# Performance work log

Measured on AMD Instinct MI355X. Metric: run time of the kernel, lower is better.

The kernel has to match this reference:

```python
import jax, jax.numpy as jnp
import numpy as np

N_NODES = 50000
N_EDGES = 1600000
IN_DIM = 64
HEADS = 8
DHEAD = 8  # out_dim per head
CLAMP = 5.0


def _xavier(key, shape):
    # xavier_normal_ for a torch Linear weight [out, in]; we store transposed [in, out]
    fan_in, fan_out = shape[0], shape[1]
    std = np.sqrt(2.0 / (fan_in + fan_out))
    return jax.random.normal(key, shape, jnp.float32) * jnp.float32(std)


def setup_inputs() -> dict:
    key = jax.random.key(0)
    ks = jax.random.split(key, 8)
    x = jax.random.normal(ks[0], (N_NODES, IN_DIM), jnp.float32)
    edge_attr = jax.random.normal(ks[1], (N_EDGES, IN_DIM), jnp.float32)
    edge_index = jax.random.randint(ks[2], (2, N_EDGES), 0, N_NODES)
    HD = HEADS * DHEAD
    WQ = _xavier(ks[3], (IN_DIM, HD)); bQ = jnp.zeros((HD,), jnp.float32)
    WK = _xavier(ks[4], (IN_DIM, HD))  # use_bias=False -> no bias for K
    WV = _xavier(ks[5], (IN_DIM, HD))  # no bias for V
    WE1 = _xavier(ks[6], (IN_DIM, HD)); bE1 = jnp.zeros((HD,), jnp.float32)
    return {"x": x, "edge_attr": edge_attr, "WQ": WQ, "bQ": bQ, "WK": WK,
            "WV": WV, "WE1": WE1, "bE1": bE1, "edge_index": edge_index}


def _segment_softmax(s, seg, num_segments):
    # pyg_softmax: numerically-stable softmax over edges grouped by destination node
    m = jax.ops.segment_max(s, seg, num_segments=num_segments)
    m = jnp.where(jnp.isfinite(m), m, jnp.float32(0.0))  # empty segments -> 0
    e = jnp.exp(s - m[seg])
    den = jax.ops.segment_sum(e, seg, num_segments=num_segments)
    return e / (den[seg] + jnp.float32(1e-16))


def _forward(x, edge_attr, WQ, bQ, WK, WV, WE1, bE1, edge_index):
    Q = (x @ WQ + bQ).reshape(N_NODES, HEADS, DHEAD)
    K = (x @ WK).reshape(N_NODES, HEADS, DHEAD)
    V = (x @ WV).reshape(N_NODES, HEADS, DHEAD)
    E = (edge_attr @ WE1 + bE1).reshape(N_EDGES, HEADS, DHEAD)
    src, dst = edge_index[0], edge_index[1]
    # score = K[src] * Q[dst]; score_e = score * E  (attn_product='mul', act=Identity)
    score_e = K[src] * Q[dst] * E                  # [Ne, H, D]
    wE = score_e.reshape(N_EDGES, HEADS * DHEAD)   # edge output
    s = score_e.sum(-1, keepdims=True) / jnp.sqrt(jnp.float32(DHEAD))  # [Ne, H, 1]
    s = jnp.clip(s, -CLAMP, CLAMP)
    alpha = _segment_softmax(s, dst, N_NODES)      # [Ne, H, 1]
    msg = V[src] * alpha
    wV = jax.ops.segment_sum(msg, dst, num_segments=N_NODES)
    # edge_enhance (edge_reweight=False): add segment-sum of score_e * alpha
    wV = wV + jax.ops.segment_sum(score_e * alpha, dst, num_segments=N_NODES)
    return wV, wE


def reference(x, edge_attr, WQ, bQ, WK, WV, WE1, bE1, edge_index):
    return _forward(x, edge_attr, WQ, bQ, WK, WV, WE1, bE1, edge_index)
```

## Files before the change

kernel.cpp:

```cpp
#include <hip/hip_runtime.h>

#define NN 50000
#define NE 1600000
#define CLAMP_V 5.0f
#define NB 2048
#define CH ((NE + NB - 1) / NB)
#define BSHIFT 9
#define NBUCK ((NN + (1 << BSHIFT) - 1) >> BSHIFT)
#define BPAD 128

typedef __attribute__((ext_vector_type(4))) short bf16x4;
typedef __attribute__((ext_vector_type(4))) float f32x4;

static __device__ __forceinline__ short f2bf(float x) {
    unsigned u = __builtin_bit_cast(unsigned, x);
    u += 0x7FFF + ((u >> 16) & 1);
    return (short)(u >> 16);
}

__global__ __launch_bounds__(256) void proj_kernel(
    const float* __restrict__ x,
    const float* __restrict__ WQ, const float* __restrict__ bQ,
    const float* __restrict__ WK, const float* __restrict__ WVw,
    float* __restrict__ Q, float* __restrict__ K, float* __restrict__ V)
{
    __shared__ float sWQ[4096], sWK[4096], sWV[4096];
    for (int i = threadIdx.x; i < 4096; i += 256) {
        sWQ[i] = WQ[i]; sWK[i] = WK[i]; sWV[i] = WVw[i];
    }
    __syncthreads();
    const int col = threadIdx.x & 63;
    const int nl  = threadIdx.x >> 6;
    const float bq = bQ[col];
    for (int node = blockIdx.x * 4 + nl; node < NN; node += gridDim.x * 4) {
        const float* xr = x + (size_t)node * 64;
        float aq = 0.f, ak = 0.f, av = 0.f;
        #pragma unroll
        for (int j = 0; j < 64; ++j) {
            float xv = xr[j];
            aq = fmaf(xv, sWQ[j*64+col], aq);
            ak = fmaf(xv, sWK[j*64+col], ak);
            av = fmaf(xv, sWV[j*64+col], av);
        }
        Q[(size_t)node*64+col] = aq + bq;
        K[(size_t)node*64+col] = ak;
        V[(size_t)node*64+col] = av;
    }
}

__global__ __launch_bounds__(256) void hist1_kernel(
    const int* __restrict__ ei, int* __restrict__ blockHist)
{
    __shared__ int h[BPAD];
    if (threadIdx.x < BPAD) h[threadIdx.x] = 0;
    __syncthreads();
    const int b  = blockIdx.x;
    const int e0 = b * CH;
    const int e1 = (e0 + CH < NE) ? e0 + CH : NE;
    for (int e = e0 + threadIdx.x; e < e1; e += 256)
        atomicAdd(&h[ei[NE + e] >> BSHIFT], 1);
    __syncthreads();
    if (threadIdx.x < NBUCK) blockHist[b * BPAD + threadIdx.x] = h[threadIdx.x];
}

__global__ __launch_bounds__(64) void scanA_kernel(
    int* __restrict__ blockHist, int* __restrict__ bucketTotal)
{
    const int k    = blockIdx.x;
    const int lane = threadIdx.x;
    int running = 0;
    for (int c = 0; c < NB; c += 64) {
        int v = blockHist[(c + lane) * BPAD + k];
        int incl = v;
        #pragma unroll
        for (int d = 1; d < 64; d <<= 1) {
            int t = __shfl_up(incl, d);
            if (lane >= d) incl += t;
        }
        blockHist[(c + lane) * BPAD + k] = running + (incl - v);
        running += __shfl(incl, 63);
    }
    if (lane == 0) bucketTotal[k] = running;
}

__global__ void scanB_kernel(const int* __restrict__ bucketTotal,
                             int* __restrict__ bucketStart)
{
    int acc = 0;
    for (int k = 0; k < NBUCK; ++k) { bucketStart[k] = acc; acc += bucketTotal[k]; }
    bucketStart[NBUCK] = acc;
}

__global__ __launch_bounds__(256) void scatter1_kernel(
    const int* __restrict__ ei, const int* __restrict__ blockHist,
    const int* __restrict__ bucketStart, uint2* __restrict__ binned)
{
    __shared__ int cur[BPAD];
    const int b = blockIdx.x;
    if (threadIdx.x < NBUCK)
        cur[threadIdx.x] = bucketStart[threadIdx.x] + blockHist[b * BPAD + threadIdx.x];
    __syncthreads();
    const int e0 = b * CH;
    const int e1 = (e0 + CH < NE) ? e0 + CH : NE;
    for (int e = e0 + threadIdx.x; e < e1; e += 256) {
        const unsigned src = ei[e], dst = ei[NE + e];
        const int pos = atomicAdd(&cur[dst >> BSHIFT], 1);
        binned[pos] = make_uint2((dst << 16) | src, (unsigned)e);
    }
}

__global__ __launch_bounds__(1024) void sort2_kernel(
    const uint2* __restrict__ binned, const int* __restrict__ bucketStart,
    uint2* __restrict__ sorted)
{
    __shared__ int cnt[512];
    __shared__ int pre[512];
    const int b  = blockIdx.x;
    const int lo = bucketStart[b];
    const int hi = bucketStart[b + 1];
    if (threadIdx.x < 512) cnt[threadIdx.x] = 0;
    __syncthreads();
    for (int p = lo + threadIdx.x; p < hi; p += 1024)
        atomicAdd(&cnt[(binned[p].x >> 16) & 511], 1);
    __syncthreads();
    if (threadIdx.x < 512) pre[threadIdx.x] = cnt[threadIdx.x];
    __syncthreads();
    for (int d = 1; d < 512; d <<= 1) {
        int t = (threadIdx.x < 512 && threadIdx.x >= d) ? pre[threadIdx.x - d] : 0;
        __syncthreads();
        if (threadIdx.x < 512) pre[threadIdx.x] += t;
        __syncthreads();
    }
    if (threadIdx.x < 512)
        cnt[threadIdx.x] = lo + pre[threadIdx.x] - cnt[threadIdx.x];
    __syncthreads();
    for (int p = lo + threadIdx.x; p < hi; p += 1024) {
        const uint2 q = binned[p];
        const int pos = atomicAdd(&cnt[(q.x >> 16) & 511], 1);
        sorted[pos] = q;
    }
}

__global__ __launch_bounds__(256) void edge_fused_kernel(
    const float* __restrict__ edge_attr,
    const float* __restrict__ WE1, const float* __restrict__ bE1,
    const uint2* __restrict__ sorted,
    const float* __restrict__ Q, const float* __restrict__ K,
    const float* __restrict__ V,
    float* __restrict__ wE, float* __restrict__ den, float* __restrict__ Num)
{
    __shared__ float Elds[4][16 * 64];
    __shared__ float exL[4][16 * 8];
    __shared__ int   dstL[4][16];
    const int tid  = threadIdx.x;
    const int wv   = tid >> 6;
    const int lane = tid & 63;
    const int g    = lane >> 4;
    const int rowl = lane & 15;

    bf16x4 bF[4][4];
    float  bias[4];
    #pragma unroll
    for (int cb = 0; cb < 4; ++cb) {
        const int col = rowl + 16 * cb;
        bias[cb] = bE1[col];
        #pragma unroll
        for (int ks = 0; ks < 4; ++ks) {
            bf16x4 t;
            #pragma unroll
            for (int j = 0; j < 4; ++j)
                t[j] = f2bf(WE1[(ks * 16 + g * 4 + j) * 64 + col]);
            bF[cb][ks] = t;
        }
    }

    const float inv_sqrt8 = 0.35355339059327373f;

    for (int tile = blockIdx.x; tile < (NE / 64); tile += gridDim.x) {
        const int pBase = tile * 64 + wv * 16;

        const uint2 qv  = sorted[pBase + rowl];
        const int  srcv = qv.x & 0xffff;
        const int  dstv = qv.x >> 16;
        const int  eidv = (int)qv.y;
        if (lane < 16) dstL[wv][lane] = dstv;

        bf16x4 aF[4];
        const float* ar = edge_attr + (size_t)eidv * 64 + g * 4;
        #pragma unroll
        for (int ks = 0; ks < 4; ++ks) {
            f32x4 v = __builtin_nontemporal_load(
                reinterpret_cast<const f32x4*>(ar + ks * 16));
            bf16x4 t;
            #pragma unroll
            for (int j = 0; j < 4; ++j) t[j] = f2bf(v[j]);
            aF[ks] = t;
        }

        f32x4 acc[4];
        #pragma unroll
        for (int cb = 0; cb < 4; ++cb) {
            acc[cb][0] = bias[cb]; acc[cb][1] = bias[cb];
            acc[cb][2] = bias[cb]; acc[cb][3] = bias[cb];
        }
        #pragma unroll
        for (int cb = 0; cb < 4; ++cb)
            #pragma unroll
            for (int ks = 0; ks < 4; ++ks)
                acc[cb] = __builtin_amdgcn_mfma_f32_16x16x16bf16_1k(
                    aF[ks], bF[cb][ks], acc[cb], 0, 0, 0);

        #pragma unroll
        for (int cb = 0; cb < 4; ++cb)
            #pragma unroll
            for (int r = 0; r < 4; ++r)
                Elds[wv][(g * 4 + r) * 64 + rowl + 16 * cb] = acc[cb][r];

        #pragma unroll
        for (int qi = 0; qi < 4; ++qi) {
            const int el  = qi * 4 + g;
            const int eid = __shfl(eidv, el);
            const int src = __shfl(srcv, el);
            const int dst = __shfl(dstv, el);
            const f32x4 Kv = *reinterpret_cast<const f32x4*>(K + (size_t)src * 64 + rowl * 4);
            const f32x4 Qv = *reinterpret_cast<const f32x4*>(Q + (size_t)dst * 64 + rowl * 4);
            const f32x4 Vv = *reinterpret_cast<const f32x4*>(V + (size_t)src * 64 + rowl * 4);
            f32x4* eslot = reinterpret_cast<f32x4*>(&Elds[wv][el * 64 + rowl * 4]);
            const f32x4 El = *eslot;
            f32x4 sc;
            #pragma unroll
            for (int j = 0; j < 4; ++j) sc[j] = Kv[j] * Qv[j] * El[j];
            __builtin_nontemporal_store(sc,
                reinterpret_cast<f32x4*>(wE + (size_t)eid * 64 + rowl * 4));
            float ss = sc[0] + sc[1] + sc[2] + sc[3];
            ss += __shfl_xor(ss, 1);
            float s = fminf(fmaxf(ss * inv_sqrt8, -CLAMP_V), CLAMP_V);
            float ex = __expf(s);
            if ((rowl & 1) == 0)
                exL[wv][el * 8 + (rowl >> 1)] = ex;
            f32x4 t;
            #pragma unroll
            for (int j = 0; j < 4; ++j) t[j] = ex * (Vv[j] + sc[j]);
            *eslot = t;
        }

        float accP = 0.f, accD = 0.f;
        int cur = dstL[wv][0];
        #pragma unroll
        for (int el = 0; el < 16; ++el) {
            accP += Elds[wv][el * 64 + lane];
            accD += exL[wv][el * 8 + (lane & 7)];
            const int nxt = (el < 15) ? dstL[wv][el + 1] : -1;
            if (nxt != cur) {
                atomicAdd(&Num[(size_t)cur * 64 + lane], accP);
                if (lane < 8) atomicAdd(&den[cur * 8 + lane], accD);
                accP = 0.f; accD = 0.f; cur = nxt;
            }
        }
    }
}

__global__ __launch_bounds__(256) void finalize_kernel(
    const float* __restrict__ Num, const float* __restrict__ den,
    float* __restrict__ wV)
{
    const int i = blockIdx.x * 256 + threadIdx.x;
    if (i >= NN * 16) return;
    const int c4 = i & 15;
    const int n  = i >> 4;
    const int h  = c4 >> 1;
    const float d = den[n * 8 + h] + 1e-16f;
    f32x4 v = reinterpret_cast<const f32x4*>(Num)[i];
    v[0] /= d; v[1] /= d; v[2] /= d; v[3] /= d;
    reinterpret_cast<f32x4*>(wV)[i] = v;
}

extern "C" void kernel_launch(void* const* d_in, const int* in_sizes, int n_in,
                              void* d_out, int out_size, void* d_ws, size_t ws_size,
                              hipStream_t stream) {
    const float* x         = (const float*)d_in[0];
    const float* edge_attr = (const float*)d_in[1];
    const float* WQ        = (const float*)d_in[2];
    const float* bQ        = (const float*)d_in[3];
    const float* WK        = (const float*)d_in[4];
    const float* WVw       = (const float*)d_in[5];
    const float* WE1       = (const float*)d_in[6];
    const float* bE1       = (const float*)d_in[7];
    const int*   ei        = (const int*)d_in[8];

    float* out = (float*)d_out;
    float* wV = out;
    float* wE = out + (size_t)NN * 64;

    float* Q           = (float*)d_ws;
    float* K           = Q + (size_t)NN * 64;
    float* V           = K + (size_t)NN * 64;
    float* den         = V + (size_t)NN * 64;
    float* Num         = den + (size_t)NN * 8;
    int*   blockHist   = (int*)(Num + (size_t)NN * 64);
    int*   bucketTotal = blockHist + NB * BPAD;
    int*   bucketStart = bucketTotal + BPAD;
    uint2* binned      = (uint2*)(bucketStart + BPAD);
    uint2* sorted      = binned + NE;

    hipMemsetAsync(den, 0, (size_t)NN * (8 + 64) * sizeof(float), stream);

    hist1_kernel<<<NB, 256, 0, stream>>>(ei, blockHist);
    scanA_kernel<<<NBUCK, 64, 0, stream>>>(blockHist, bucketTotal);
    scanB_kernel<<<1, 1, 0, stream>>>(bucketTotal, bucketStart);
    scatter1_kernel<<<NB, 256, 0, stream>>>(ei, blockHist, bucketStart, binned);
    sort2_kernel<<<NBUCK, 1024, 0, stream>>>(binned, bucketStart, sorted);
    proj_kernel<<<1024, 256, 0, stream>>>(x, WQ, bQ, WK, WVw, Q, K, V);
    edge_fused_kernel<<<2048, 256, 0, stream>>>(edge_attr, WE1, bE1, sorted,
                                                Q, K, V, wE, den, Num);
    finalize_kernel<<<(NN * 16 + 255) / 256, 256, 0, stream>>>(Num, den, wV);
}
```

Baseline: 354.5 us.

## Partition edges by CSR node ranges per wave to drop atomics and finalize pass

sort2 now emits a CSR row_ptr. Each wave binary-searches row_ptr to own a contiguous, node-aligned range of sorted edges, so every destination node is fully reduced inside one wave. The wave writes wV directly as accP/(accD+eps), which removes the atomicAdds into Num/den, the zeroing memset of those buffers and the separate finalize kernel. The cost is uneven per-wave work because ranges end on node boundaries, partial 16-edge tiles with masking, and a binary search at the start of each wave.

```diff
diff --git a/kernel.cpp b/kernel.cpp
--- a/kernel.cpp
+++ b/kernel.cpp
@@ -84,11 +84,13 @@
 }
 
 __global__ void scanB_kernel(const int* __restrict__ bucketTotal,
-                             int* __restrict__ bucketStart)
+                             int* __restrict__ bucketStart,
+                             int* __restrict__ row_ptr)
 {
     int acc = 0;
     for (int k = 0; k < NBUCK; ++k) { bucketStart[k] = acc; acc += bucketTotal[k]; }
     bucketStart[NBUCK] = acc;
+    row_ptr[NN] = acc;
 }
 
 __global__ __launch_bounds__(256) void scatter1_kernel(
@@ -111,7 +113,7 @@
 
 __global__ __launch_bounds__(1024) void sort2_kernel(
     const uint2* __restrict__ binned, const int* __restrict__ bucketStart,
-    uint2* __restrict__ sorted)
+    uint2* __restrict__ sorted, int* __restrict__ row_ptr)
 {
     __shared__ int cnt[512];
     __shared__ int pre[512];
@@ -131,8 +133,11 @@
         if (threadIdx.x < 512) pre[threadIdx.x] += t;
         __syncthreads();
     }
-    if (threadIdx.x < 512)
+    if (threadIdx.x < 512) {
         cnt[threadIdx.x] = lo + pre[threadIdx.x] - cnt[threadIdx.x];
+        const int node = (b << BSHIFT) + threadIdx.x;
+        if (node < NN) row_ptr[node] = cnt[threadIdx.x];
+    }
     __syncthreads();
     for (int p = lo + threadIdx.x; p < hi; p += 1024) {
         const uint2 q = binned[p];
@@ -141,13 +146,13 @@
     }
 }
 
-__global__ __launch_bounds__(256) void edge_fused_kernel(
+__global__ __launch_bounds__(256) void edge_csr_kernel(
     const float* __restrict__ edge_attr,
     const float* __restrict__ WE1, const float* __restrict__ bE1,
-    const uint2* __restrict__ sorted,
+    const uint2* __restrict__ sorted, const int* __restrict__ row_ptr,
     const float* __restrict__ Q, const float* __restrict__ K,
     const float* __restrict__ V,
-    float* __restrict__ wE, float* __restrict__ den, float* __restrict__ Num)
+    float* __restrict__ wE, float* __restrict__ wV)
 {
     __shared__ float Elds[4][16 * 64];
     __shared__ float exL[4][16 * 8];
@@ -174,12 +179,27 @@
         }
     }
 
+    const int NW = gridDim.x * 4;
+    const int w  = blockIdx.x * 4 + wv;
+    const int t0 = (int)((long long)NE * w / NW);
+    const int t1 = (int)((long long)NE * (w + 1) / NW);
+    int lo = 0, hi = NN;
+    while (lo < hi) { int m = (lo + hi) >> 1; if (row_ptr[m] < t0) lo = m + 1; else hi = m; }
+    const int nStart = lo;
+    hi = NN;
+    while (lo < hi) { int m = (lo + hi) >> 1; if (row_ptr[m] < t1) lo = m + 1; else hi = m; }
+    const int eS = row_ptr[nStart];
+    const int eE = row_ptr[lo];
+
     const float inv_sqrt8 = 0.35355339059327373f;
-
-    for (int tile = blockIdx.x; tile < (NE / 64); tile += gridDim.x) {
-        const int pBase = tile * 64 + wv * 16;
-
-        const uint2 qv  = sorted[pBase + rowl];
+    float accP = 0.f, accD = 0.f;
+    int   cur  = -1;
+
+    for (int base = eS; base < eE; base += 16) {
+        const int cnt16 = (eE - base < 16) ? (eE - base) : 16;
+
+        const int  p    = base + (rowl < cnt16 ? rowl : cnt16 - 1);
+        const uint2 qv  = sorted[p];
         const int  srcv = qv.x & 0xffff;
         const int  dstv = qv.x >> 16;
         const int  eidv = (int)qv.y;
@@ -218,61 +238,61 @@
 
         #pragma unroll
         for (int qi = 0; qi < 4; ++qi) {
-            const int el  = qi * 4 + g;
-            const int eid = __shfl(eidv, el);
-            const int src = __shfl(srcv, el);
-            const int dst = __shfl(dstv, el);
-            const f32x4 Kv = *reinterpret_cast<const f32x4*>(K + (size_t)src * 64 + rowl * 4);
-            const f32x4 Qv = *reinterpret_cast<const f32x4*>(Q + (size_t)dst * 64 + rowl * 4);
-            const f32x4 Vv = *reinterpret_cast<const f32x4*>(V + (size_t)src * 64 + rowl * 4);
-            f32x4* eslot = reinterpret_cast<f32x4*>(&Elds[wv][el * 64 + rowl * 4]);
-            const f32x4 El = *eslot;
-            f32x4 sc;
-            #pragma unroll
-            for (int j = 0; j < 4; ++j) sc[j] = Kv[j] * Qv[j] * El[j];
-            __builtin_nontemporal_store(sc,
-                reinterpret_cast<f32x4*>(wE + (size_t)eid * 64 + rowl * 4));
-            float ss = sc[0] + sc[1] + sc[2] + sc[3];
-            ss += __shfl_xor(ss, 1);
-            float s = fminf(fmaxf(ss * inv_sqrt8, -CLAMP_V), CLAMP_V);
-            float ex = __expf(s);
-            if ((rowl & 1) == 0)
-                exL[wv][el * 8 + (rowl >> 1)] = ex;
-            f32x4 t;
-            #pragma unroll
-            for (int j = 0; j < 4; ++j) t[j] = ex * (Vv[j] + sc[j]);
-            *eslot = t;
-        }
-
-        float accP = 0.f, accD = 0.f;
-        int cur = dstL[wv][0];
-        #pragma unroll
-        for (int el = 0; el < 16; ++el) {
-            accP += Elds[wv][el * 64 + lane];
-            accD += exL[wv][el * 8 + (lane & 7)];
-            const int nxt = (el < 15) ? dstL[wv][el + 1] : -1;
-            if (nxt != cur) {
-                atomicAdd(&Num[(size_t)cur * 64 + lane], accP);
-                if (lane < 8) atomicAdd(&den[cur * 8 + lane], accD);
-                accP = 0.f; accD = 0.f; cur = nxt;
+            const int el = qi * 4 + g;
+            if (el < cnt16) {
+                const int eid = __shfl(eidv, el);
+                const int src = __shfl(srcv, el);
+                const int dst = __shfl(dstv, el);
+                const f32x4 Kv = *reinterpret_cast<const f32x4*>(K + (size_t)src * 64 + rowl * 4);
+                const f32x4 Qv = *reinterpret_cast<const f32x4*>(Q + (size_t)dst * 64 + rowl * 4);
+                const f32x4 Vv = *reinterpret_cast<const f32x4*>(V + (size_t)src * 64 + rowl * 4);
+                f32x4* eslot = reinterpret_cast<f32x4*>(&Elds[wv][el * 64 + rowl * 4]);
+                const f32x4 El = *eslot;
+                f32x4 sc;
+                #pragma unroll
+                for (int j = 0; j < 4; ++j) sc[j] = Kv[j] * Qv[j] * El[j];
+                __builtin_nontemporal_store(sc,
+                    reinterpret_cast<f32x4*>(wE + (size_t)eid * 64 + rowl * 4));
+                float ss = sc[0] + sc[1] + sc[2] + sc[3];
+                ss += __shfl_xor(ss, 1);
+                float s = fminf(fmaxf(ss * inv_sqrt8, -CLAMP_V), CLAMP_V);
+                float ex = __expf(s);
+                if ((rowl & 1) == 0)
+                    exL[wv][el * 8 + (rowl >> 1)] = ex;
+                f32x4 t;
+                #pragma unroll
+                for (int j = 0; j < 4; ++j) t[j] = ex * (Vv[j] + sc[j]);
+                *eslot = t;
             }
         }
-    }
-}
-
-__global__ __launch_bounds__(256) void finalize_kernel(
-    const float* __restrict__ Num, const float* __restrict__ den,
-    float* __restrict__ wV)
-{
-    const int i = blockIdx.x * 256 + threadIdx.x;
-    if (i >= NN * 16) return;
-    const int c4 = i & 15;
-    const int n  = i >> 4;
-    const int h  = c4 >> 1;
-    const float d = den[n * 8 + h] + 1e-16f;
-    f32x4 v = reinterpret_cast<const f32x4*>(Num)[i];
-    v[0] /= d; v[1] /= d; v[2] /= d; v[3] /= d;
-    reinterpret_cast<f32x4*>(wV)[i] = v;
+
+        if (cnt16 == 16) {
+            #pragma unroll
+            for (int el = 0; el < 16; ++el) {
+                const int d = dstL[wv][el];
+                if (d != cur) {
+                    if (cur >= 0)
+                        wV[(size_t)cur * 64 + lane] = accP / (accD + 1e-16f);
+                    accP = 0.f; accD = 0.f; cur = d;
+                }
+                accP += Elds[wv][el * 64 + lane];
+                accD += exL[wv][el * 8 + (lane >> 3)];
+            }
+        } else {
+            for (int el = 0; el < cnt16; ++el) {
+                const int d = dstL[wv][el];
+                if (d != cur) {
+                    if (cur >= 0)
+                        wV[(size_t)cur * 64 + lane] = accP / (accD + 1e-16f);
+                    accP = 0.f; accD = 0.f; cur = d;
+                }
+                accP += Elds[wv][el * 64 + lane];
+                accD += exL[wv][el * 8 + (lane >> 3)];
+            }
+        }
+    }
+    if (cur >= 0)
+        wV[(size_t)cur * 64 + lane] = accP / (accD + 1e-16f);
 }
 
 extern "C" void kernel_launch(void* const* d_in, const int* in_sizes, int n_in,
@@ -295,23 +315,21 @@
     float* Q           = (float*)d_ws;
     float* K           = Q + (size_t)NN * 64;
     float* V           = K + (size_t)NN * 64;
-    float* den         = V + (size_t)NN * 64;
-    float* Num         = den + (size_t)NN * 8;
-    int*   blockHist   = (int*)(Num + (size_t)NN * 64);
+    int*   row_ptr     = (int*)(V + (size_t)NN * 64);
+    int*   blockHist   = row_ptr + NN + 2;
     int*   bucketTotal = blockHist + NB * BPAD;
     int*   bucketStart = bucketTotal + BPAD;
     uint2* binned      = (uint2*)(bucketStart + BPAD);
     uint2* sorted      = binned + NE;
 
-    hipMemsetAsync(den, 0, (size_t)NN * (8 + 64) * sizeof(float), stream);
+    hipMemsetAsync(wV, 0, (size_t)NN * 64 * sizeof(float), stream);
 
     hist1_kernel<<<NB, 256, 0, stream>>>(ei, blockHist);
     scanA_kernel<<<NBUCK, 64, 0, stream>>>(blockHist, bucketTotal);
-    scanB_kernel<<<1, 1, 0, stream>>>(bucketTotal, bucketStart);
+    scanB_kernel<<<1, 1, 0, stream>>>(bucketTotal, bucketStart, row_ptr);
     scatter1_kernel<<<NB, 256, 0, stream>>>(ei, blockHist, bucketStart, binned);
-    sort2_kernel<<<NBUCK, 1024, 0, stream>>>(binned, bucketStart, sorted);
+    sort2_kernel<<<NBUCK, 1024, 0, stream>>>(binned, bucketStart, sorted, row_ptr);
     proj_kernel<<<1024, 256, 0, stream>>>(x, WQ, bQ, WK, WVw, Q, K, V);
-    edge_fused_kernel<<<2048, 256, 0, stream>>>(edge_attr, WE1, bE1, sorted,
-                                                Q, K, V, wE, den, Num);
-    finalize_kernel<<<(NN * 16 + 255) / 256, 256, 0, stream>>>(Num, den, wV);
-}
+    edge_csr_kernel<<<2048, 256, 0, stream>>>(edge_attr, WE1, bE1, sorted, row_ptr,
+                                              Q, K, V, wE, wV);
+}
```

New measurement: 397.2 us. 12.0% more time.
